# Performance work log

Hardware: AMD Instinct MI355X
Metric: run time of the kernel (lower is better)

The kernel has to match this reference:

```python
import jax, jax.numpy as jnp
import numpy as np

M = 4  # mixture size of the AttentionStem value embedding

def unfold_windows(a, kh, kw, Hout, Wout):
    # a: [..., Hp, Wp] -> [..., Hout, Wout, kh, kw] (stride-1 sliding windows, cropped)
    rows = []
    for i in range(kh):
        cols = [a[..., i:i + Hout, j:j + Wout] for j in range(kw)]
        rows.append(jnp.stack(cols, axis=-1))
    return jnp.stack(rows, axis=-2)

def attention_stem(x, qw, kw_, vw, emb_a, emb_b, emb_mix, kh, kw, pad):
    # x: [B,Cin,H,W]; qw/kw_: [Cin,Co]; vw: [M,Cin,Co]; emb_a:[Co,kh]; emb_b:[Co,kw]; emb_mix:[M,Co]
    B, Cin, H, W = x.shape
    pl, pr, pt, pb = pad  # F.pad order (left,right,top,bottom)
    xp = jnp.pad(x, ((0, 0), (0, 0), (pt, pb), (pl, pr)))
    Hp, Wp = xp.shape[2], xp.shape[3]
    Hout = min(Hp - kh + 1, H)
    Wout = min(Wp - kw + 1, W)
    q = jnp.einsum('bchw,co->bohw', x[:, :, :Hout, :Wout], qw)       # 1x1 conv query
    k = jnp.einsum('bchw,co->bohw', xp, kw_)                          # 1x1 conv key on padded
    v = jnp.einsum('bchw,mco->mbohw', xp, vw)                         # m 1x1 conv values
    k_win = unfold_windows(k, kh, kw, Hout, Wout)                     # [B,Co,Ho,Wo,kh,kw]
    v_win = unfold_windows(v, kh, kw, Hout, Wout)                     # [M,B,Co,Ho,Wo,kh,kw]
    # mixture relative-position embedding, softmax over mixtures per (kh,kw) offset
    la = emb_mix @ emb_a                                              # [M,kh]
    lb = emb_mix @ emb_b                                              # [M,kw]
    emb = jax.nn.softmax(la[:, :, None] + lb[:, None, :], axis=0)     # [M,kh,kw]
    v_agg = jnp.einsum('mkl,mbohwkl->bohwkl', emb, v_win)             # [B,Co,Ho,Wo,kh,kw]
    K = kh * kw
    scores = jnp.einsum('bohw,bohwkl->bhwkl', q, k_win).reshape(B, Hout, Wout, K)
    attn = jax.nn.softmax(scores, axis=-1).reshape(B, Hout, Wout, kh, kw)
    out = jnp.einsum('bhwkl,bohwkl->bohw', attn, v_agg)               # [B,Co,Ho,Wo]
    return out

def bn_relu(x, g, b):
    # training-mode BatchNorm2d + ReLU
    mu = x.mean(axis=(0, 2, 3), keepdims=True)
    var = x.var(axis=(0, 2, 3), keepdims=True)
    y = (x - mu) * jax.lax.rsqrt(var + 1e-5) * g[None, :, None, None] + b[None, :, None, None]
    return jax.nn.relu(y)

def _params(key):
    ks = jax.random.split(key, 18)
    def w(k, shape):
        return jax.random.normal(k, shape, dtype=jnp.float32) * 0.1
    cfg = [(1, 64, 1, 5), (64, 128, 2, 5), (128, 16, 2, 5)]
    p = {}
    i = 0
    for s, (ci, co, kh, kw) in enumerate(cfg):
        p[f'p{s}_q'] = w(ks[i], (ci, co)); i += 1
        p[f'p{s}_k'] = w(ks[i], (ci, co)); i += 1
        p[f'p{s}_v'] = w(ks[i], (M, ci, co)); i += 1
        p[f'p{s}_ea'] = w(ks[i], (co, kh)); i += 1
        p[f'p{s}_eb'] = w(ks[i], (co, kw)); i += 1
        p[f'p{s}_em'] = w(ks[i], (M, co)); i += 1
        p[f'p{s}_g'] = jnp.ones((co,), jnp.float32)
        p[f'p{s}_b'] = jnp.zeros((co,), jnp.float32)
    return p

def setup_inputs() -> dict:
    key = jax.random.key(0)
    kx, kp = jax.random.split(key)
    inp = {'x': jax.random.normal(kx, (2, 1, 8, 3000), dtype=jnp.float32)}
    inp.update(_params(kp))
    return inp

def reference(x,
              p0_q, p0_k, p0_v, p0_ea, p0_eb, p0_em, p0_g, p0_b,
              p1_q, p1_k, p1_v, p1_ea, p1_eb, p1_em, p1_g, p1_b,
              p2_q, p2_k, p2_v, p2_ea, p2_eb, p2_em, p2_g, p2_b):
    h = attention_stem(x, p0_q, p0_k, p0_v, p0_ea, p0_eb, p0_em, 1, 5, (2, 2, 0, 0))
    h = bn_relu(h, p0_g, p0_b)[:, :, ::2, ::2]                        # MaxPool2d(1,2) == stride-2 subsample
    h = attention_stem(h, p1_q, p1_k, p1_v, p1_ea, p1_eb, p1_em, 2, 5, (2, 2, 1, 1))
    h = bn_relu(h, p1_g, p1_b)[:, :, ::2, ::2]
    h = attention_stem(h, p2_q, p2_k, p2_v, p2_ea, p2_eb, p2_em, 2, 5, (2, 2, 0, 0))
    h = bn_relu(h, p2_g, p2_b)
    B, C, H, W = h.shape
    nW = W // 56                                                       # AvgPool2d((1,56))
    return h[:, :, :, :nW * 56].reshape(B, C, H, nW, 56).mean(-1)
```

## Files before the change

### kernel.cpp

```cpp
#include <hip/hip_runtime.h>
#include <math.h>


#define TPB 256

__global__ void prep0_kernel(const float* __restrict__ ea,
                             const float* __restrict__ eb,
                             const float* __restrict__ em,
                             const float* __restrict__ qw,
                             const float* __restrict__ kw_,
                             const float* __restrict__ vw,
                             float* __restrict__ par) {
    const int M4 = 4, Co = 64, kw = 5;
    __shared__ float la[4];
    __shared__ float lb[20];
    __shared__ float embs[20];
    int tid = threadIdx.x;
    if (tid < 64) {
        float p = qw[tid] * kw_[tid];
#pragma unroll
        for (int d = 1; d < 64; d <<= 1) p += __shfl_xor(p, d, 64);
        if (tid == 0) par[0] = p;
    }
    if (tid >= 64 && tid < 64 + M4) {
        int m = tid - 64;
        float s = 0.f;
        for (int o = 0; o < Co; ++o) s += em[m * Co + o] * ea[o];
        la[m] = s;
    }
    if (tid >= 128 && tid < 128 + M4 * kw) {
        int r = tid - 128;
        int m = r / kw, l = r % kw;
        float s = 0.f;
        for (int o = 0; o < Co; ++o) s += em[m * Co + o] * eb[o * kw + l];
        lb[m * kw + l] = s;
    }
    __syncthreads();
    if (tid < 5) {
        float lg[4];
        float mx = -1e30f;
        for (int m = 0; m < M4; ++m) {
            lg[m] = la[m] + lb[m * kw + tid];
            mx = fmaxf(mx, lg[m]);
        }
        float sum = 0.f;
        for (int m = 0; m < M4; ++m) { lg[m] = expf(lg[m] - mx); sum += lg[m]; }
        float inv = 1.f / sum;
        for (int m = 0; m < M4; ++m) embs[tid * 4 + m] = lg[m] * inv;
    }
    __syncthreads();
    for (int e = tid; e < 5 * 64; e += blockDim.x) {
        int t = e / 64, o = e - t * 64;
        float s = 0.f;
        for (int m = 0; m < M4; ++m) s += embs[t * 4 + m] * vw[m * 64 + o];
        par[1 + e] = s;
    }
}

__global__ void attn_out0_kernel(const float* __restrict__ x,
                                 const float* __restrict__ par,
                                 float* __restrict__ h0raw,
                                 float2* __restrict__ part0) {
    __shared__ float wsh[5][256];
    __shared__ float vsh[5 * 64];
    __shared__ float wred[4][20];
    __shared__ float wfin[20];
    int tid = threadIdx.x;
    int b = blockIdx.y;
    int oz = blockIdx.z;
    int n0 = blockIdx.x * 256;
    int n = n0 + tid;
    for (int i = tid; i < 320; i += 256) vsh[i] = par[1 + i];
    float c0 = par[0];
    float warr[5];
    if (n < 24000) {
        int h = n / 3000, w = n - h * 3000;
        const float* xr = x + b * 24000 + h * 3000;
        float xc = xr[w];
        float xs[5], s[5];
#pragma unroll
        for (int t = 0; t < 5; ++t) {
            int col = w + t - 2;
            xs[t] = (col >= 0 && col < 3000) ? xr[col] : 0.f;
            s[t] = c0 * xc * xs[t];
        }
        float mx = s[0];
#pragma unroll
        for (int t = 1; t < 5; ++t) mx = fmaxf(mx, s[t]);
        float sum = 0.f;
#pragma unroll
        for (int t = 0; t < 5; ++t) { s[t] = expf(s[t] - mx); sum += s[t]; }
        float inv = 1.f / sum;
#pragma unroll
        for (int t = 0; t < 5; ++t) warr[t] = s[t] * inv * xs[t];
    } else {
#pragma unroll
        for (int t = 0; t < 5; ++t) warr[t] = 0.f;
    }
#pragma unroll
    for (int t = 0; t < 5; ++t) wsh[t][tid] = warr[t];
    float p[20];
#pragma unroll
    for (int t = 0; t < 5; ++t) p[t] = warr[t];
    {
        int k = 5;
#pragma unroll
        for (int t = 0; t < 5; ++t)
#pragma unroll
            for (int t2 = t; t2 < 5; ++t2) p[k++] = warr[t] * warr[t2];
    }
#pragma unroll
    for (int d = 1; d < 64; d <<= 1)
#pragma unroll
        for (int i = 0; i < 20; ++i) p[i] += __shfl_xor(p[i], d, 64);
    if ((tid & 63) == 0)
#pragma unroll
        for (int i = 0; i < 20; ++i) wred[tid >> 6][i] = p[i];
    __syncthreads();
    if (tid < 20)
        wfin[tid] = wred[0][tid] + wred[1][tid] + wred[2][tid] + wred[3][tid];
    __syncthreads();
    int jq = tid & 63, og = tid >> 6;
    int nq = n0 + jq * 4;
    int h = nq / 3000, w0 = nq - h * 3000;
    bool st = (nq < 24000) && ((h & 1) == 0);
    float wq[5][4];
#pragma unroll
    for (int t = 0; t < 5; ++t)
#pragma unroll
        for (int j = 0; j < 4; ++j) wq[t][j] = wsh[t][jq * 4 + j];
    int obase = oz * 32 + og * 8;
    for (int oi = 0; oi < 8; ++oi) {
        int o = obase + oi;
        float4 v = make_float4(0.f, 0.f, 0.f, 0.f);
#pragma unroll
        for (int t = 0; t < 5; ++t) {
            float vo = vsh[t * 64 + o];
            v.x = fmaf(wq[t][0], vo, v.x);
            v.y = fmaf(wq[t][1], vo, v.y);
            v.z = fmaf(wq[t][2], vo, v.z);
            v.w = fmaf(wq[t][3], vo, v.w);
        }
        if (st) {
            size_t base = ((size_t)b * 64 + o) * 6000 + (h >> 1) * 1500 + (w0 >> 1);
            *(float2*)&h0raw[base] = make_float2(v.x, v.z);
        }
    }
    if (tid < 32) {
        int o = oz * 32 + tid;
        float vt[5];
#pragma unroll
        for (int t = 0; t < 5; ++t) vt[t] = vsh[t * 64 + o];
        float s = 0.f, s2 = 0.f;
#pragma unroll
        for (int t = 0; t < 5; ++t) s = fmaf(vt[t], wfin[t], s);
        int k = 5;
#pragma unroll
        for (int t = 0; t < 5; ++t)
#pragma unroll
            for (int t2 = t; t2 < 5; ++t2) {
                float coef = (t == t2) ? vt[t] * vt[t] : 2.f * vt[t] * vt[t2];
                s2 = fmaf(coef, wfin[k], s2);
                ++k;
            }
        int chunk = b * gridDim.x + blockIdx.x;
        part0[(size_t)o * 188 + chunk] = make_float2(s, s2);
    }
}

__global__ void prep_stage1_kernel(const float* __restrict__ ea,
                                   const float* __restrict__ eb,
                                   const float* __restrict__ em,
                                   const float* __restrict__ qw,
                                   const float* __restrict__ kw_,
                                   const float* __restrict__ vw,
                                   float* __restrict__ G,
                                   float* __restrict__ Av,
                                   const float2* __restrict__ part0,
                                   float* __restrict__ mr0) {
    const int M4 = 4, Co = 128, kh = 2, kw = 5, Cin = 64;
    __shared__ float la[8];
    __shared__ float lb[20];
    __shared__ float embs[40];
    int tid = threadIdx.x;
    if (blockIdx.x == 0 && tid < 64) {
        double s = 0.0, s2 = 0.0;
        for (int i = 0; i < 188; ++i) {
            float2 p = part0[(size_t)tid * 188 + i];
            s += p.x; s2 += p.y;
        }
        double mean = s / 48000.0;
        double var = s2 / 48000.0 - mean * mean;
        mr0[tid] = (float)mean;
        mr0[64 + tid] = (float)(1.0 / sqrt(var + 1e-5));
    }
    if (tid < M4 * kh) {
        int m = tid / kh, k = tid % kh;
        float s = 0.f;
        for (int o = 0; o < Co; ++o) s += em[m * Co + o] * ea[o * kh + k];
        la[tid] = s;
    }
    if (tid >= 64 && tid < 64 + M4 * kw) {
        int r = tid - 64;
        int m = r / kw, l = r % kw;
        float s = 0.f;
        for (int o = 0; o < Co; ++o) s += em[m * Co + o] * eb[o * kw + l];
        lb[r] = s;
    }
    __syncthreads();
    if (tid < 10) {
        int k = tid / kw, l = tid % kw;
        float lg[4];
        float mx = -1e30f;
        for (int m = 0; m < M4; ++m) {
            lg[m] = la[m * kh + k] + lb[m * kw + l];
            mx = fmaxf(mx, lg[m]);
        }
        float sum = 0.f;
        for (int m = 0; m < M4; ++m) { lg[m] = expf(lg[m] - mx); sum += lg[m]; }
        float inv = 1.f / sum;
        for (int m = 0; m < M4; ++m) embs[tid * 4 + m] = lg[m] * inv;
    }
    __syncthreads();
    const int TOTG = 64 * 64;
    const int TOT2 = 640 * 128;
    int nth = gridDim.x * blockDim.x;
    for (int e = blockIdx.x * blockDim.x + tid; e < TOTG + TOT2; e += nth) {
        if (e < TOTG) {
            int c = e >> 6, c2 = e & 63;
            float s = 0.f;
            for (int o = 0; o < 128; ++o)
                s = fmaf(qw[c * 128 + o], kw_[c2 * 128 + o], s);
            G[e] = s;
        } else {
            int e2 = e - TOTG;
            int k = e2 / Co, o = e2 - k * Co;
            int c = k / 10, t = k - c * 10;
            float val = 0.f;
            for (int m = 0; m < M4; ++m)
                val += embs[t * 4 + m] * vw[(m * Cin + c) * Co + o];
            Av[e2] = val;
        }
    }
}

__global__ void prep_wcat_kernel(const float* __restrict__ ea,
                                 const float* __restrict__ eb,
                                 const float* __restrict__ em,
                                 const float* __restrict__ qw,
                                 const float* __restrict__ kw_,
                                 const float* __restrict__ vw,
                                 float* __restrict__ Wcat,
                                 int Co, int kh, int kw, int Cin,
                                 const float2* __restrict__ part,
                                 float* __restrict__ mr,
                                 int Cprev, int NCH, int count) {
    const int M4 = 4;
    __shared__ float la[8];
    __shared__ float lb[20];
    __shared__ float embs[40];
    int K = kh * kw;
    int tid = threadIdx.x;
    if (blockIdx.x == 0 && tid < Cprev) {
        double s = 0.0, s2 = 0.0;
        for (int i = 0; i < NCH; ++i) {
            float2 p = part[(size_t)tid * NCH + i];
            s += p.x; s2 += p.y;
        }
        double mean = s / count;
        double var = s2 / count - mean * mean;
        mr[tid] = (float)mean;
        mr[Cprev + tid] = (float)(1.0 / sqrt(var + 1e-5));
    }
    if (tid < M4 * kh) {
        int m = tid / kh, k = tid % kh;
        float s = 0.f;
        for (int o = 0; o < Co; ++o) s += em[m * Co + o] * ea[o * kh + k];
        la[tid] = s;
    }
    if (tid >= 64 && tid < 64 + M4 * kw) {
        int r = tid - 64;
        int m = r / kw, l = r % kw;
        float s = 0.f;
        for (int o = 0; o < Co; ++o) s += em[m * Co + o] * eb[o * kw + l];
        lb[r] = s;
    }
    __syncthreads();
    if (tid < K) {
        int k = tid / kw, l = tid % kw;
        float lg[4];
        float mx = -1e30f;
        for (int m = 0; m < M4; ++m) {
            lg[m] = la[m * kh + k] + lb[m * kw + l];
            mx = fmaxf(mx, lg[m]);
        }
        float sum = 0.f;
        for (int m = 0; m < M4; ++m) { lg[m] = expf(lg[m] - mx); sum += lg[m]; }
        float inv = 1.f / sum;
        for (int m = 0; m < M4; ++m) embs[tid * 4 + m] = lg[m] * inv;
    }
    __syncthreads();
    int Mtot = (2 + K) * Co;
    long long total = (long long)Mtot * Cin;
    for (long long e = (long long)blockIdx.x * blockDim.x + tid; e < total;
         e += (long long)gridDim.x * blockDim.x) {
        int m = (int)(e / Cin);
        int c = (int)(e - (long long)m * Cin);
        float val;
        if (m < Co) {
            val = qw[c * Co + m];
        } else if (m < 2 * Co) {
            val = kw_[c * Co + (m - Co)];
        } else {
            int mz = m - 2 * Co;
            int t = mz / Co;
            int o = mz - t * Co;
            val = 0.f;
            for (int mm = 0; mm < M4; ++mm)
                val += embs[t * 4 + mm] * vw[(mm * Cin + c) * Co + o];
        }
        Wcat[e] = val;
    }
}

__global__ void attn_v4_kernel(const float* __restrict__ G,
                               const float* __restrict__ xraw,
                               const float* __restrict__ mr,
                               const float* __restrict__ g,
                               const float* __restrict__ bb,
                               float* __restrict__ attn) {
    __shared__ float xw[64][2][68];
    __shared__ float gbuf[64][64];
    __shared__ float ssh[64][12];
    __shared__ float scb[64], sfb[64];
    int tid = threadIdx.x;
    int chunk = blockIdx.x;
    int ho = blockIdx.y;
    int b = blockIdx.z;
    int wo0 = chunk * 64;
    if (tid < 64) {
        float sc = mr[64 + tid] * g[tid];
        scb[tid] = sc;
        sfb[tid] = bb[tid] - mr[tid] * sc;
    }
    for (int e = tid; e < 4096; e += 256)
        gbuf[e >> 6][e & 63] = G[e];
    __syncthreads();
    for (int e = tid; e < 64 * 136; e += 256) {
        int c = e / 136;
        int r2 = e - c * 136;
        int r = r2 / 68, jj = r2 - r * 68;
        int row = ho - 1 + r;
        int col = wo0 + jj - 2;
        float v = 0.f;
        if (row >= 0 && col >= 0 && col < 1500) {
            float xv = xraw[((size_t)b * 64 + c) * 6000 + row * 1500 + col];
            v = fmaxf(fmaf(xv, scb[c], sfb[c]), 0.f);
        }
        xw[c][r][jj] = v;
    }
    __syncthreads();
    int j = tid & 63, cg = tid >> 6;
    float ul[16];
#pragma unroll
    for (int i = 0; i < 16; ++i) ul[i] = 0.f;
    for (int c = 0; c < 64; ++c) {
        float xv = xw[c][1][j + 2];
        float4 g0 = *(const float4*)&gbuf[c][cg * 16 + 0];
        float4 g1 = *(const float4*)&gbuf[c][cg * 16 + 4];
        float4 g2 = *(const float4*)&gbuf[c][cg * 16 + 8];
        float4 g3 = *(const float4*)&gbuf[c][cg * 16 + 12];
        ul[0]  = fmaf(g0.x, xv, ul[0]);  ul[1]  = fmaf(g0.y, xv, ul[1]);
        ul[2]  = fmaf(g0.z, xv, ul[2]);  ul[3]  = fmaf(g0.w, xv, ul[3]);
        ul[4]  = fmaf(g1.x, xv, ul[4]);  ul[5]  = fmaf(g1.y, xv, ul[5]);
        ul[6]  = fmaf(g1.z, xv, ul[6]);  ul[7]  = fmaf(g1.w, xv, ul[7]);
        ul[8]  = fmaf(g2.x, xv, ul[8]);  ul[9]  = fmaf(g2.y, xv, ul[9]);
        ul[10] = fmaf(g2.z, xv, ul[10]); ul[11] = fmaf(g2.w, xv, ul[11]);
        ul[12] = fmaf(g3.x, xv, ul[12]); ul[13] = fmaf(g3.y, xv, ul[13]);
        ul[14] = fmaf(g3.z, xv, ul[14]); ul[15] = fmaf(g3.w, xv, ul[15]);
    }
    __syncthreads();
#pragma unroll
    for (int i = 0; i < 16; ++i) gbuf[cg * 16 + i][j] = ul[i];
    __syncthreads();
    int t0 = cg, t1 = cg + 4, t2 = cg + 8;
    int dk0 = t0 / 5, dl0 = t0 % 5;
    int dk1 = t1 / 5, dl1 = t1 % 5;
    int dk2 = (t2 < 10) ? 1 : 0, dl2 = (t2 < 10) ? (t2 - 5) : 0;
    float s0 = 0.f, s1 = 0.f, s2v = 0.f;
    for (int c = 0; c < 64; ++c) {
        float uv = gbuf[c][j];
        s0 = fmaf(uv, xw[c][dk0][j + dl0], s0);
        s1 = fmaf(uv, xw[c][dk1][j + dl1], s1);
        if (t2 < 10) s2v = fmaf(uv, xw[c][dk2][j + dl2], s2v);
    }
    ssh[j][t0] = s0;
    ssh[j][t1] = s1;
    if (t2 < 10) ssh[j][t2] = s2v;
    __syncthreads();
    if (tid < 64 && wo0 + tid < 1500) {
        float sc[10];
        float mx = -1e30f;
#pragma unroll
        for (int t = 0; t < 10; ++t) { sc[t] = ssh[tid][t]; mx = fmaxf(mx, sc[t]); }
        float sum = 0.f;
#pragma unroll
        for (int t = 0; t < 10; ++t) { sc[t] = expf(sc[t] - mx); sum += sc[t]; }
        float inv = 1.f / sum;
        int n = ho * 1500 + wo0 + tid;
#pragma unroll
        for (int t = 0; t < 10; ++t)
            attn[((size_t)b * 10 + t) * 6000 + n] = sc[t] * inv;
    }
}

__launch_bounds__(256)
__global__ void vgemm_kernel(const float* __restrict__ Av,
                             const float* __restrict__ xraw,
                             const float* __restrict__ attn,
                             const float* __restrict__ mr,
                             const float* __restrict__ g,
                             const float* __restrict__ bb,
                             float* __restrict__ partial) {
    __shared__ float Bs[20][64];
    __shared__ float xw[16][2][68];
    __shared__ float att_s[10][64];
    __shared__ float scl[16], sfl[16];
    int tid = threadIdx.x;
    int nt = blockIdx.x;
    int ho = nt / 24, chunk = nt - ho * 24;
    int wo0 = chunk * 64;
    int sk = blockIdx.y;
    int b = blockIdx.z;
    int c_base = sk * 16;
    int lane = tid & 63;
    int wq = tid >> 6;
    int wqu = __builtin_amdgcn_readfirstlane(wq);
    if (tid < 16) {
        int c = c_base + tid;
        float sc = mr[64 + c] * g[c];
        scl[tid] = sc;
        sfl[tid] = bb[c] - mr[c] * sc;
    }
    __syncthreads();
    for (int e = tid; e < 16 * 136; e += 256) {
        int c = e / 136;
        int r2 = e - c * 136;
        int r = r2 / 68, jj = r2 - r * 68;
        int row = ho - 1 + r;
        int col = wo0 + jj - 2;
        float v = 0.f;
        if (row >= 0 && col >= 0 && col < 1500) {
            float xv = xraw[((size_t)b * 64 + c_base + c) * 6000 + row * 1500 + col];
            v = fmaxf(fmaf(xv, scl[c], sfl[c]), 0.f);
        }
        xw[c][r][jj] = v;
    }
    for (int e = tid; e < 640; e += 256) {
        int t = e >> 6, jj = e & 63;
        int col = wo0 + jj;
        att_s[t][jj] = (col < 1500)
            ? attn[((size_t)b * 10 + t) * 6000 + ho * 1500 + col] : 0.f;
    }
    __syncthreads();
    float acc[32];
#pragma unroll
    for (int i = 0; i < 32; ++i) acc[i] = 0.f;
    int dk = wq & 1;
    int clh = wq >> 1;
    for (int kc = 0; kc < 8; ++kc) {
#pragma unroll
        for (int it = 0; it < 5; ++it)
            Bs[wq * 5 + it][lane] =
                xw[kc * 2 + clh][dk][lane + it] * att_s[dk * 5 + it][lane];
        __syncthreads();
        const float* ap0 = Av + (size_t)(c_base * 10 + kc * 20) * 128 + wqu * 32;
#pragma unroll
        for (int kk = 0; kk < 20; ++kk) {
            float bv = Bs[kk][lane];
            const float* ap = ap0 + kk * 128;
#pragma unroll
            for (int i = 0; i < 32; ++i)
                acc[i] = fmaf(ap[i], bv, acc[i]);
        }
        __syncthreads();
    }
    int wo = wo0 + lane;
    if (wo < 1500) {
        int n = ho * 1500 + wo;
#pragma unroll
        for (int i = 0; i < 32; ++i) {
            int o = wq * 32 + i;
            partial[(((size_t)sk * 2 + b) * 128 + o) * 6000 + n] = acc[i];
        }
    }
}

__global__ void vreduce_kernel(const float* __restrict__ partial,
                               float* __restrict__ h1raw,
                               float2* __restrict__ part1) {
    int tid = threadIdx.x;
    int by = blockIdx.y;
    int b = by >> 7, o = by & 127;
    int n = blockIdx.x * 1024 + tid * 4;
    float4 v = make_float4(0.f, 0.f, 0.f, 0.f);
    if (n < 6000) {
#pragma unroll
        for (int sk = 0; sk < 4; ++sk) {
            float4 p = *(const float4*)&partial[(((size_t)sk * 2 + b) * 128 + o) * 6000 + n];
            v.x += p.x; v.y += p.y; v.z += p.z; v.w += p.w;
        }
        int ho = n / 1500, wo = n - ho * 1500;
        if ((ho & 1) == 0) {
            size_t base = ((size_t)b * 128 + o) * 1500 + (ho >> 1) * 750 + (wo >> 1);
            *(float2*)&h1raw[base] = make_float2(v.x, v.z);
        }
    }
    float s = v.x + v.y + v.z + v.w;
    float s2 = v.x * v.x + v.y * v.y + v.z * v.z + v.w * v.w;
    __shared__ float sh[TPB], sh2[TPB];
    sh[tid] = s; sh2[tid] = s2;
    __syncthreads();
    for (int st = TPB / 2; st > 0; st >>= 1) {
        if (tid < st) { sh[tid] += sh[tid + st]; sh2[tid] += sh2[tid + st]; }
        __syncthreads();
    }
    if (tid == 0)
        part1[(size_t)o * 12 + b * 6 + blockIdx.x] = make_float2(sh[0], sh2[0]);
}

__launch_bounds__(256, 4)
__global__ void gemm_qkbn_kernel(const float* __restrict__ A,
                                 const float* __restrict__ xraw,
                                 const float* __restrict__ mr,
                                 const float* __restrict__ g,
                                 const float* __restrict__ bb,
                                 float* __restrict__ qk,
                                 float* __restrict__ z,
                                 int M, int N, int K, int twoCo) {
    __shared__ float As[32][132];
    __shared__ float Bs[32][132];
    __shared__ float scale[128], shift[128];
    int tid = threadIdx.x;
    int b = blockIdx.z;
    int m0 = blockIdx.y * 128, n0 = blockIdx.x * 128;
    int Mz = M - twoCo;
    float acc[8][8] = {{0.f}};
    int am = tid >> 1, ak = (tid & 1) * 16;
    int bk = tid >> 3, bn = (tid & 7) * 16;
    int tm = tid & 15, tn = tid >> 4;
    for (int c = tid; c < K; c += 256) {
        float sc = mr[K + c] * g[c];
        scale[c] = sc;
        shift[c] = bb[c] - mr[c] * sc;
    }
    __syncthreads();
    for (int k0 = 0; k0 < K; k0 += 32) {
        {
            int mA = m0 + am;
            const float* Ap = A + (size_t)mA * K + k0 + ak;
#pragma unroll
            for (int q = 0; q < 4; ++q) {
                float4 v = (mA < M) ? *(const float4*)(Ap + q * 4)
                                    : make_float4(0.f, 0.f, 0.f, 0.f);
                int kk = ak + q * 4;
                As[kk + 0][am] = v.x;
                As[kk + 1][am] = v.y;
                As[kk + 2][am] = v.z;
                As[kk + 3][am] = v.w;
            }
        }
        {
            int c = k0 + bk;
            float sc = scale[c], sf = shift[c];
            const float* Xp = xraw + ((size_t)b * K + c) * N + n0 + bn;
            if (n0 + 128 <= N) {
#pragma unroll
                for (int q = 0; q < 4; ++q) {
                    float4 v = *(const float4*)(Xp + q * 4);
                    v.x = fmaxf(fmaf(v.x, sc, sf), 0.f);
                    v.y = fmaxf(fmaf(v.y, sc, sf), 0.f);
                    v.z = fmaxf(fmaf(v.z, sc, sf), 0.f);
                    v.w = fmaxf(fmaf(v.w, sc, sf), 0.f);
                    *(float4*)&Bs[bk][bn + q * 4] = v;
                }
            } else {
#pragma unroll
                for (int q = 0; q < 16; ++q) {
                    int n = n0 + bn + q;
                    Bs[bk][bn + q] = (n < N) ? fmaxf(fmaf(Xp[q], sc, sf), 0.f) : 0.f;
                }
            }
        }
        __syncthreads();
#pragma unroll 8
        for (int k = 0; k < 32; ++k) {
            float4 a0 = *(const float4*)&As[k][tm * 4];
            float4 a1 = *(const float4*)&As[k][64 + tm * 4];
            float4 b0 = *(const float4*)&Bs[k][tn * 4];
            float4 b1 = *(const float4*)&Bs[k][64 + tn * 4];
            float av[8] = {a0.x, a0.y, a0.z, a0.w, a1.x, a1.y, a1.z, a1.w};
            float bv[8] = {b0.x, b0.y, b0.z, b0.w, b1.x, b1.y, b1.z, b1.w};
#pragma unroll
            for (int i = 0; i < 8; ++i)
#pragma unroll
                for (int j = 0; j < 8; ++j)
                    acc[i][j] = fmaf(av[i], bv[j], acc[i][j]);
        }
        __syncthreads();
    }
    bool fullN = (n0 + 128 <= N);
#pragma unroll
    for (int iq = 0; iq < 2; ++iq) {
        int mb = m0 + iq * 64 + tm * 4;
        if (mb >= M) continue;
        if (mb < twoCo) {
#pragma unroll
            for (int jq = 0; jq < 2; ++jq)
#pragma unroll
                for (int jj = 0; jj < 4; ++jj) {
                    int n = n0 + jq * 64 + tn * 4 + jj;
                    if (n < N) {
                        float4 v = make_float4(acc[iq * 4 + 0][jq * 4 + jj],
                                               acc[iq * 4 + 1][jq * 4 + jj],
                                               acc[iq * 4 + 2][jq * 4 + jj],
                                               acc[iq * 4 + 3][jq * 4 + jj]);
                        *(float4*)&qk[((size_t)b * N + n) * twoCo + mb] = v;
                    }
                }
        } else {
#pragma unroll
            for (int i = 0; i < 4; ++i) {
                int row = mb + i - twoCo;
                float* zp = &z[((size_t)b * Mz + row) * N];
#pragma unroll
                for (int jq = 0; jq < 2; ++jq) {
                    int nb_ = n0 + jq * 64 + tn * 4;
                    if (fullN) {
                        *(float4*)&zp[nb_] = make_float4(acc[iq * 4 + i][jq * 4 + 0],
                                                         acc[iq * 4 + i][jq * 4 + 1],
                                                         acc[iq * 4 + i][jq * 4 + 2],
                                                         acc[iq * 4 + i][jq * 4 + 3]);
                    } else {
#pragma unroll
                        for (int jj = 0; jj < 4; ++jj)
                            if (nb_ + jj < N) zp[nb_ + jj] = acc[iq * 4 + i][jq * 4 + jj];
                    }
                }
            }
        }
    }
}

template <int KH, int KW, int CO, int NPB>
__global__ void attn_v3_kernel(const float* __restrict__ qk,
                               float* __restrict__ attn,
                               int H, int W, int Ho, int Wo, int pt, int pl) {
    const int K = KH * KW;
    __shared__ float ssh[NPB][K];
    int tid = threadIdx.x;
    int b = blockIdx.y;
    int ln = tid / K, t = tid - ln * K;
    int Nout = Ho * Wo;
    int n = blockIdx.x * NPB + ln;
    bool active = (tid < NPB * K) && (n < Nout);
    int HWin = H * W;
    float sv = 0.f;
    if (active) {
        int ho = n / Wo, wo = n - ho * Wo;
        int row = ho + t / KW - pt, col = wo + t % KW - pl;
        if (row >= 0 && row < H && col >= 0 && col < W) {
            const float* qp = qk + ((size_t)b * HWin + ho * W + wo) * (2 * CO);
            const float* kp = qk + ((size_t)b * HWin + (size_t)row * W + col) * (2 * CO) + CO;
#pragma unroll
            for (int o = 0; o < CO; o += 4) {
                float4 q4 = *(const float4*)(qp + o);
                float4 k4 = *(const float4*)(kp + o);
                sv += q4.x * k4.x + q4.y * k4.y + q4.z * k4.z + q4.w * k4.w;
            }
        }
        ssh[ln][t] = sv;
    }
    __syncthreads();
    if (active) {
        float mx = ssh[ln][0];
#pragma unroll
        for (int tt = 1; tt < K; ++tt) mx = fmaxf(mx, ssh[ln][tt]);
        float sum = 0.f;
#pragma unroll
        for (int tt = 0; tt < K; ++tt) sum += expf(ssh[ln][tt] - mx);
        float num = expf(sv - mx);
        attn[((size_t)b * K + t) * Nout + n] = num / sum;
    }
}

template <int KH, int KW>
__global__ void combine_stats_kernel(const float* __restrict__ z,
                                     const float* __restrict__ attn,
                                     float* __restrict__ out,
                                     float2* __restrict__ part,
                                     int Co, int Mz,
                                     int H, int W, int Ho, int Wo,
                                     int pt, int pl) {
    const int K = KH * KW;
    int tid = threadIdx.x;
    int bc = blockIdx.y;
    int b = bc / Co, o = bc - b * Co;
    int Nout = Ho * Wo, Nin = H * W;
    int n = blockIdx.x * blockDim.x + tid;
    float val = 0.f;
    if (n < Nout) {
        int ho = n / Wo, wo = n - ho * Wo;
#pragma unroll
        for (int dk = 0; dk < KH; ++dk) {
            int row = ho + dk - pt;
            if (row < 0 || row >= H) continue;
#pragma unroll
            for (int dl = 0; dl < KW; ++dl) {
                int col = wo + dl - pl;
                if (col < 0 || col >= W) continue;
                int t = dk * KW + dl;
                float a = attn[((size_t)b * K + t) * Nout + n];
                float zv = z[((size_t)b * Mz + t * Co + o) * Nin + row * W + col];
                val = fmaf(a, zv, val);
            }
        }
        out[((size_t)b * Co + o) * Nout + n] = val;
    }
    __shared__ float sh[TPB], sh2[TPB];
    sh[tid] = (n < Nout) ? val : 0.f;
    sh2[tid] = (n < Nout) ? val * val : 0.f;
    __syncthreads();
    for (int st = TPB / 2; st > 0; st >>= 1) {
        if (tid < st) { sh[tid] += sh[tid + st]; sh2[tid] += sh2[tid + st]; }
        __syncthreads();
    }
    if (tid == 0) {
        int chunk = b * gridDim.x + blockIdx.x;
        part[(size_t)o * (2 * gridDim.x) + chunk] = make_float2(sh[0], sh2[0]);
    }
}

__global__ void bn_avg_final_kernel(const float* __restrict__ x,
                                    const float2* __restrict__ part,
                                    const float* __restrict__ g,
                                    const float* __restrict__ bb,
                                    float* __restrict__ out,
                                    int B, int C, int W, int nW, int NCH) {
    int idx = blockIdx.x * blockDim.x + threadIdx.x;
    int N = B * C * nW;
    if (idx >= N) return;
    int j = idx % nW; int r = idx / nW;
    int c = r % C; int b = r / C;
    double s = 0.0, s2 = 0.0;
    for (int i = 0; i < NCH; ++i) {
        float2 p = part[(size_t)c * NCH + i];
        s += p.x; s2 += p.y;
    }
    double cnt = (double)B * W;
    double mean = s / cnt;
    double var = s2 / cnt - mean * mean;
    float rstd = (float)(1.0 / sqrt(var + 1e-5));
    float meanf = (float)mean, gg = g[c], bo = bb[c];
    const float* xb = x + ((long long)b * C + c) * W + j * 56;
    float acc = 0.f;
    for (int i = 0; i < 56; ++i) {
        float yn = (xb[i] - meanf) * rstd * gg + bo;
        acc += fmaxf(yn, 0.f);
    }
    out[idx] = acc * (1.f / 56.f);
}

extern "C" void kernel_launch(void* const* d_in, const int* in_sizes, int n_in,
                              void* d_out, int out_size, void* d_ws, size_t ws_size,
                              hipStream_t stream) {
    const float* x   = (const float*)d_in[0];
    const float* qw0 = (const float*)d_in[1];
    const float* kw0 = (const float*)d_in[2];
    const float* vw0 = (const float*)d_in[3];
    const float* ea0 = (const float*)d_in[4];
    const float* eb0 = (const float*)d_in[5];
    const float* em0 = (const float*)d_in[6];
    const float* g0  = (const float*)d_in[7];
    const float* b0  = (const float*)d_in[8];
    const float* qw1 = (const float*)d_in[9];
    const float* kw1 = (const float*)d_in[10];
    const float* vw1 = (const float*)d_in[11];
    const float* ea1 = (const float*)d_in[12];
    const float* eb1 = (const float*)d_in[13];
    const float* em1 = (const float*)d_in[14];
    const float* g1  = (const float*)d_in[15];
    const float* b1  = (const float*)d_in[16];
    const float* qw2 = (const float*)d_in[17];
    const float* kw2 = (const float*)d_in[18];
    const float* vw2 = (const float*)d_in[19];
    const float* ea2 = (const float*)d_in[20];
    const float* eb2 = (const float*)d_in[21];
    const float* em2 = (const float*)d_in[22];
    const float* g2  = (const float*)d_in[23];
    const float* b2  = (const float*)d_in[24];
    float* outp = (float*)d_out;
    (void)ws_size; (void)in_sizes; (void)n_in; (void)out_size;

    float* ws = (float*)d_ws;
    size_t off = 0;
    auto alloc = [&](size_t n) { float* p = ws + off; off += (n + 63) & ~(size_t)63; return p; };

    float* par0   = alloc(321);
    float* part0  = alloc(64 * 188 * 2);
    float* mr0    = alloc(128);
    float* h0raw  = alloc(2 * 64 * 6000);
    float* G1     = alloc(64 * 64);
    float* Av1    = alloc(640 * 128);
    float* attn1  = alloc(2 * 10 * 6000);
    float* vpart  = alloc(4 * 2 * 128 * 6000);
    float* part1  = alloc(128 * 12 * 2);
    float* mr1    = alloc(256);
    float* h1raw  = alloc(2 * 128 * 1500);
    float* Wcat2  = alloc(192 * 128);
    float* qk2    = alloc(2 * 1500 * 32);
    float* z2     = alloc(2 * 160 * 1500);
    float* attn2  = alloc(2 * 10 * 750);
    float* part2  = alloc(16 * 6 * 2);
    float* s2     = alloc(2 * 16 * 750);

    auto grid = [](int n) { return (n + TPB - 1) / TPB; };

    prep0_kernel<<<1, TPB, 0, stream>>>(ea0, eb0, em0, qw0, kw0, vw0, par0);
    {
        dim3 g(94, 2, 2);
        attn_out0_kernel<<<g, TPB, 0, stream>>>(x, par0, h0raw, (float2*)part0);
    }
    prep_stage1_kernel<<<64, TPB, 0, stream>>>(ea1, eb1, em1, qw1, kw1, vw1,
        G1, Av1, (const float2*)part0, mr0);
    {
        dim3 g(24, 4, 2);
        attn_v4_kernel<<<g, TPB, 0, stream>>>(G1, h0raw, mr0, g0, b0, attn1);
    }
    {
        dim3 g(96, 4, 2);
        vgemm_kernel<<<g, TPB, 0, stream>>>(Av1, h0raw, attn1, mr0, g0, b0, vpart);
    }
    {
        dim3 g(6, 256);
        vreduce_kernel<<<g, TPB, 0, stream>>>(vpart, h1raw, (float2*)part1);
    }
    prep_wcat_kernel<<<24, TPB, 0, stream>>>(ea2, eb2, em2, qw2, kw2, vw2, Wcat2,
        16, 2, 5, 128, (const float2*)part1, mr1, 128, 12, 12000);
    {
        dim3 g(12, 2, 2);
        gemm_qkbn_kernel<<<g, TPB, 0, stream>>>(Wcat2, h1raw, mr1, g1, b1,
            qk2, z2, 192, 1500, 128, 32);
    }
    {
        dim3 g(750 / 25, 2);
        attn_v3_kernel<2, 5, 16, 25><<<g, TPB, 0, stream>>>(qk2, attn2,
            2, 750, 1, 750, 0, 2);
    }
    {
        dim3 g(3, 2 * 16);
        combine_stats_kernel<2, 5><<<g, TPB, 0, stream>>>(z2, attn2, s2,
            (float2*)part2, 16, 160, 2, 750, 1, 750, 0, 2);
    }
    bn_avg_final_kernel<<<grid(2 * 16 * 13), TPB, 0, stream>>>(s2, (const float2*)part2,
        g2, b2, outp, 2, 16, 750, 13, 6);
}
```

Before: 257.5 us.

## Restructure stage-1 value path as plain 1x1 GEMM then windowed combine

Stage 1 no longer folds the attention weights into the GEMM's B operand (vgemm with K=640 plus a split-K reduction). It now computes all four mixture value projections with the existing gemm_qkbn kernel (512x6000x64 per batch). A new combine kernel then applies attention times the mixture embedding over the 2x5 window and also gathers BN statistics. The aim is to shrink the GEMM reduction dimension and drop the split-K partial buffer, at the cost of writing and re-reading a large 2x512x6000 intermediate.

```diff
diff --git a/kernel.cpp b/kernel.cpp
--- a/kernel.cpp
+++ b/kernel.cpp
@@ -175,10 +175,11 @@
                                    const float* __restrict__ kw_,
                                    const float* __restrict__ vw,
                                    float* __restrict__ G,
-                                   float* __restrict__ Av,
+                                   float* __restrict__ Wy,
+                                   float* __restrict__ embs1,
                                    const float2* __restrict__ part0,
                                    float* __restrict__ mr0) {
-    const int M4 = 4, Co = 128, kh = 2, kw = 5, Cin = 64;
+    const int M4 = 4, Co = 128, kh = 2, kw = 5;
     __shared__ float la[8];
     __shared__ float lb[20];
     __shared__ float embs[40];
@@ -222,10 +223,11 @@
         for (int m = 0; m < M4; ++m) embs[tid * 4 + m] = lg[m] * inv;
     }
     __syncthreads();
+    if (blockIdx.x == 0 && tid < 40) embs1[tid] = embs[tid];
     const int TOTG = 64 * 64;
-    const int TOT2 = 640 * 128;
+    const int TOTW = 512 * 64;
     int nth = gridDim.x * blockDim.x;
-    for (int e = blockIdx.x * blockDim.x + tid; e < TOTG + TOT2; e += nth) {
+    for (int e = blockIdx.x * blockDim.x + tid; e < TOTG + TOTW; e += nth) {
         if (e < TOTG) {
             int c = e >> 6, c2 = e & 63;
             float s = 0.f;
@@ -234,12 +236,9 @@
             G[e] = s;
         } else {
             int e2 = e - TOTG;
-            int k = e2 / Co, o = e2 - k * Co;
-            int c = k / 10, t = k - c * 10;
-            float val = 0.f;
-            for (int m = 0; m < M4; ++m)
-                val += embs[t * 4 + m] * vw[(m * Cin + c) * Co + o];
-            Av[e2] = val;
+            int r = e2 >> 6, c = e2 & 63;
+            int m = r >> 7, o = r & 127;
+            Wy[e2] = vw[(m * 64 + c) * 128 + o];
         }
     }
 }
@@ -412,121 +411,6 @@
         for (int t = 0; t < 10; ++t)
             attn[((size_t)b * 10 + t) * 6000 + n] = sc[t] * inv;
     }
-}
-
-__launch_bounds__(256)
-__global__ void vgemm_kernel(const float* __restrict__ Av,
-                             const float* __restrict__ xraw,
-                             const float* __restrict__ attn,
-                             const float* __restrict__ mr,
-                             const float* __restrict__ g,
-                             const float* __restrict__ bb,
-                             float* __restrict__ partial) {
-    __shared__ float Bs[20][64];
-    __shared__ float xw[16][2][68];
-    __shared__ float att_s[10][64];
-    __shared__ float scl[16], sfl[16];
-    int tid = threadIdx.x;
-    int nt = blockIdx.x;
-    int ho = nt / 24, chunk = nt - ho * 24;
-    int wo0 = chunk * 64;
-    int sk = blockIdx.y;
-    int b = blockIdx.z;
-    int c_base = sk * 16;
-    int lane = tid & 63;
-    int wq = tid >> 6;
-    int wqu = __builtin_amdgcn_readfirstlane(wq);
-    if (tid < 16) {
-        int c = c_base + tid;
-        float sc = mr[64 + c] * g[c];
-        scl[tid] = sc;
-        sfl[tid] = bb[c] - mr[c] * sc;
-    }
-    __syncthreads();
-    for (int e = tid; e < 16 * 136; e += 256) {
-        int c = e / 136;
-        int r2 = e - c * 136;
-        int r = r2 / 68, jj = r2 - r * 68;
-        int row = ho - 1 + r;
-        int col = wo0 + jj - 2;
-        float v = 0.f;
-        if (row >= 0 && col >= 0 && col < 1500) {
-            float xv = xraw[((size_t)b * 64 + c_base + c) * 6000 + row * 1500 + col];
-            v = fmaxf(fmaf(xv, scl[c], sfl[c]), 0.f);
-        }
-        xw[c][r][jj] = v;
-    }
-    for (int e = tid; e < 640; e += 256) {
-        int t = e >> 6, jj = e & 63;
-        int col = wo0 + jj;
-        att_s[t][jj] = (col < 1500)
-            ? attn[((size_t)b * 10 + t) * 6000 + ho * 1500 + col] : 0.f;
-    }
-    __syncthreads();
-    float acc[32];
-#pragma unroll
-    for (int i = 0; i < 32; ++i) acc[i] = 0.f;
-    int dk = wq & 1;
-    int clh = wq >> 1;
-    for (int kc = 0; kc < 8; ++kc) {
-#pragma unroll
-        for (int it = 0; it < 5; ++it)
-            Bs[wq * 5 + it][lane] =
-                xw[kc * 2 + clh][dk][lane + it] * att_s[dk * 5 + it][lane];
-        __syncthreads();
-        const float* ap0 = Av + (size_t)(c_base * 10 + kc * 20) * 128 + wqu * 32;
-#pragma unroll
-        for (int kk = 0; kk < 20; ++kk) {
-            float bv = Bs[kk][lane];
-            const float* ap = ap0 + kk * 128;
-#pragma unroll
-            for (int i = 0; i < 32; ++i)
-                acc[i] = fmaf(ap[i], bv, acc[i]);
-        }
-        __syncthreads();
-    }
-    int wo = wo0 + lane;
-    if (wo < 1500) {
-        int n = ho * 1500 + wo;
-#pragma unroll
-        for (int i = 0; i < 32; ++i) {
-            int o = wq * 32 + i;
-            partial[(((size_t)sk * 2 + b) * 128 + o) * 6000 + n] = acc[i];
-        }
-    }
-}
-
-__global__ void vreduce_kernel(const float* __restrict__ partial,
-                               float* __restrict__ h1raw,
-                               float2* __restrict__ part1) {
-    int tid = threadIdx.x;
-    int by = blockIdx.y;
-    int b = by >> 7, o = by & 127;
-    int n = blockIdx.x * 1024 + tid * 4;
-    float4 v = make_float4(0.f, 0.f, 0.f, 0.f);
-    if (n < 6000) {
-#pragma unroll
-        for (int sk = 0; sk < 4; ++sk) {
-            float4 p = *(const float4*)&partial[(((size_t)sk * 2 + b) * 128 + o) * 6000 + n];
-            v.x += p.x; v.y += p.y; v.z += p.z; v.w += p.w;
-        }
-        int ho = n / 1500, wo = n - ho * 1500;
-        if ((ho & 1) == 0) {
-            size_t base = ((size_t)b * 128 + o) * 1500 + (ho >> 1) * 750 + (wo >> 1);
-            *(float2*)&h1raw[base] = make_float2(v.x, v.z);
-        }
-    }
-    float s = v.x + v.y + v.z + v.w;
-    float s2 = v.x * v.x + v.y * v.y + v.z * v.z + v.w * v.w;
-    __shared__ float sh[TPB], sh2[TPB];
-    sh[tid] = s; sh2[tid] = s2;
-    __syncthreads();
-    for (int st = TPB / 2; st > 0; st >>= 1) {
-        if (tid < st) { sh[tid] += sh[tid + st]; sh2[tid] += sh2[tid + st]; }
-        __syncthreads();
-    }
-    if (tid == 0)
-        part1[(size_t)o * 12 + b * 6 + blockIdx.x] = make_float2(sh[0], sh2[0]);
 }
 
 __launch_bounds__(256, 4)
@@ -649,6 +533,67 @@
                 }
             }
         }
+    }
+}
+
+__global__ void combine1_kernel(const float* __restrict__ y,
+                                const float* __restrict__ attn,
+                                const float* __restrict__ embs1,
+                                float* __restrict__ h1raw,
+                                float2* __restrict__ part1) {
+    __shared__ float yw[4][2][256];
+    __shared__ float embl[40];
+    __shared__ float sh[TPB], sh2[TPB];
+    int tid = threadIdx.x;
+    int bx = blockIdx.x;
+    int ho = bx / 6, wc = bx - ho * 6;
+    int wo0 = wc * 250;
+    int by = blockIdx.y;
+    int b = by >> 7, o = by & 127;
+    if (tid < 40) embl[tid] = embs1[tid];
+    for (int e = tid; e < 4 * 2 * 256; e += 256) {
+        int m = e >> 9;
+        int rem = e & 511;
+        int r = rem >> 8, j = rem & 255;
+        int row = ho - 1 + r;
+        int col = wo0 - 2 + j;
+        float v = 0.f;
+        if (j < 254 && row >= 0 && row < 4 && col >= 0 && col < 1500)
+            v = y[((size_t)b * 512 + m * 128 + o) * 6000 + row * 1500 + col];
+        yw[m][r][j] = v;
+    }
+    __syncthreads();
+    float val = 0.f;
+    int wo = wo0 + tid;
+    if (tid < 250) {
+        int n = ho * 1500 + wo;
+        float a[10];
+#pragma unroll
+        for (int t = 0; t < 10; ++t)
+            a[t] = attn[((size_t)b * 10 + t) * 6000 + n];
+#pragma unroll
+        for (int m = 0; m < 4; ++m) {
+#pragma unroll
+            for (int dk = 0; dk < 2; ++dk)
+#pragma unroll
+                for (int dl = 0; dl < 5; ++dl) {
+                    int t = dk * 5 + dl;
+                    val = fmaf(a[t] * embl[t * 4 + m], yw[m][dk][tid + dl], val);
+                }
+        }
+        if (((ho | wo) & 1) == 0)
+            h1raw[((size_t)b * 128 + o) * 1500 + (ho >> 1) * 750 + (wo >> 1)] = val;
+    }
+    sh[tid] = (tid < 250) ? val : 0.f;
+    sh2[tid] = (tid < 250) ? val * val : 0.f;
+    __syncthreads();
+    for (int st = TPB / 2; st > 0; st >>= 1) {
+        if (tid < st) { sh[tid] += sh[tid + st]; sh2[tid] += sh2[tid + st]; }
+        __syncthreads();
+    }
+    if (tid == 0) {
+        int chunk = b * 24 + bx;
+        part1[(size_t)o * 48 + chunk] = make_float2(sh[0], sh2[0]);
     }
 }
 
@@ -811,10 +756,11 @@
     float* mr0    = alloc(128);
     float* h0raw  = alloc(2 * 64 * 6000);
     float* G1     = alloc(64 * 64);
-    float* Av1    = alloc(640 * 128);
+    float* Wy1    = alloc(512 * 64);
+    float* embs1  = alloc(40);
     float* attn1  = alloc(2 * 10 * 6000);
-    float* vpart  = alloc(4 * 2 * 128 * 6000);
-    float* part1  = alloc(128 * 12 * 2);
+    float* ybuf   = alloc(2 * 512 * 6000);
+    float* part1  = alloc(128 * 48 * 2);
     float* mr1    = alloc(256);
     float* h1raw  = alloc(2 * 128 * 1500);
     float* Wcat2  = alloc(192 * 128);
@@ -832,21 +778,23 @@
         attn_out0_kernel<<<g, TPB, 0, stream>>>(x, par0, h0raw, (float2*)part0);
     }
     prep_stage1_kernel<<<64, TPB, 0, stream>>>(ea1, eb1, em1, qw1, kw1, vw1,
-        G1, Av1, (const float2*)part0, mr0);
+        G1, Wy1, embs1, (const float2*)part0, mr0);
     {
         dim3 g(24, 4, 2);
         attn_v4_kernel<<<g, TPB, 0, stream>>>(G1, h0raw, mr0, g0, b0, attn1);
     }
     {
-        dim3 g(96, 4, 2);
-        vgemm_kernel<<<g, TPB, 0, stream>>>(Av1, h0raw, attn1, mr0, g0, b0, vpart);
+        dim3 g(47, 4, 2);
+        gemm_qkbn_kernel<<<g, TPB, 0, stream>>>(Wy1, h0raw, mr0, g0, b0,
+            ybuf , ybuf, 512, 6000, 64, 0);
     }
     {
-        dim3 g(6, 256);
-        vreduce_kernel<<<g, TPB, 0, stream>>>(vpart, h1raw, (float2*)part1);
+        dim3 g(24, 256);
+        combine1_kernel<<<g, TPB, 0, stream>>>(ybuf, attn1, embs1,
+            h1raw, (float2*)part1);
     }
     prep_wcat_kernel<<<24, TPB, 0, stream>>>(ea2, eb2, em2, qw2, kw2, vw2, Wcat2,
-        16, 2, 5, 128, (const float2*)part1, mr1, 128, 12, 12000);
+        16, 2, 5, 128, (const float2*)part1, mr1, 128, 48, 12000);
     {
         dim3 g(12, 2, 2);
         gemm_qkbn_kernel<<<g, TPB, 0, stream>>>(Wcat2, h1raw, mr1, g1, b1,
```

New measurement: 259.9 us. About the same (+1.0%).
